# Kernel optimization log

Hardware: AMD Instinct MI355X
Metric: run time of the kernel (lower is better)

Reference implementation:

```python
import jax, jax.numpy as jnp
import numpy as np

N = 100000          # nodes
E = 1600000         # edges
IN_DIM = 128
HID = 64
N_CLASSES = 40
N_GAT_LAYERS = 2    # n_layers - 1
ALPHA = 0.2         # LeakyReLU slope
NEG_BIG = -9.0e15


def setup_inputs() -> dict:
    key = jax.random.key(0)
    ks = jax.random.split(key, 8)
    x = jax.random.normal(ks[0], (N, IN_DIM), dtype=jnp.float32)
    edge_index = jax.random.randint(ks[1], (2, E), 0, N, dtype=jnp.int64)
    # parameters (xavier-ish scale)
    emb_w = jax.random.normal(ks[2], (IN_DIM, HID), dtype=jnp.float32) * (1.414 / np.sqrt(IN_DIM + HID))
    emb_b = jnp.zeros((HID,), dtype=jnp.float32)
    Ws = jax.random.normal(ks[3], (N_GAT_LAYERS, HID, HID), dtype=jnp.float32) * (1.414 / np.sqrt(2 * HID))
    attn_a = jax.random.normal(ks[4], (N_GAT_LAYERS, 1, 2 * HID), dtype=jnp.float32) * (1.414 / np.sqrt(1 + 2 * HID))
    out_w = jax.random.normal(ks[5], (HID, N_CLASSES), dtype=jnp.float32) * (1.414 / np.sqrt(HID + N_CLASSES))
    out_b = jnp.zeros((N_CLASSES,), dtype=jnp.float32)
    return {"x": x, "edge_index": edge_index, "emb_w": emb_w, "emb_b": emb_b,
            "Ws": Ws, "attn_a": attn_a, "out_w": out_w, "out_b": out_b}


def _gat_conv(x, edge_src, edge_dst, W, a):
    # x: [N, d_in], W: [d_in, d_out], a: [1, 2*d_out]
    wh = x @ W                                   # [N, d_out]
    d = wh.shape[1]
    a_src = a[0, :d]                             # [d]
    a_dst = a[0, d:]                             # [d]
    # (a * cat(wh[src], wh[dst])).sum(1) == (wh @ a_src)[src] + (wh @ a_dst)[dst]
    s_src = wh @ a_src                           # [N]
    s_dst = wh @ a_dst                           # [N]
    e = jax.nn.leaky_relu(s_src[edge_src] + s_dst[edge_dst], negative_slope=ALPHA)  # [E]
    att = jnp.where(e > 0, e, NEG_BIG)
    att = jax.nn.softmax(att, axis=0)            # GLOBAL softmax over all edges (as in source)
    # scatter-aggregate weighted neighbor features into destination nodes
    msgs = att[:, None] * wh[edge_src]           # [E, d_out]
    h_prime = jax.ops.segment_sum(msgs, edge_dst, num_segments=wh.shape[0])  # [N, d_out]
    return jax.nn.elu(h_prime)                   # concat=True branch


def reference(x, edge_index, emb_w, emb_b, Ws, attn_a, out_w, out_b):
    edge_src = edge_index[0]
    edge_dst = edge_index[1]
    h = x @ emb_w + emb_b                        # emb Linear
    for l in range(N_GAT_LAYERS):
        h = _gat_conv(h, edge_src, edge_dst, Ws[l], attn_a[l])
    h = h @ out_w + out_b                        # out_att Linear
    h = jax.nn.elu(h)
    return jax.nn.log_softmax(h, axis=1)
```

## Files before the change

kernel.cpp:

```cpp
#include <hip/hip_runtime.h>
#include <hip/hip_bf16.h>

#define NODES   100000
#define EDGES   1600000
#define INDIM   128
#define HID     64
#define NCLS    40
#define NEG_BIG_F (-9000000000000000.0f)
#define SENTINEL  (-3.0e38f)

#define BN       512
#define NBUCK    196
#define CHUNK    7168
#define NCHUNK   ((EDGES + CHUNK - 1) / CHUNK)
#define BCAP     8960
#define MZPB     256
#define SMB      128

using bf16x8 = __attribute__((ext_vector_type(8))) short;
using f32x4  = __attribute__((ext_vector_type(4))) float;

static __device__ __forceinline__ float b2f(__hip_bfloat16 h){
    return __bfloat162float(h);
}
static __device__ __forceinline__ float bits2f(unsigned int b){
    union { unsigned int u; float f; } v; v.u = b << 16; return v.f;
}
static __device__ __forceinline__ unsigned short f2b(float f){
    __hip_bfloat16 h = __float2bfloat16(f);
    return *reinterpret_cast<unsigned short*>(&h);
}
static __device__ __forceinline__ float ldin(const void* p, int i, bool f32){
    return f32 ? ((const float*)p)[i] : b2f(((const __hip_bfloat16*)p)[i]);
}
static __device__ __forceinline__ float elu_fast(float x){
    return (x > 0.f) ? x : (__expf(x) - 1.f);
}
static __device__ __forceinline__ unsigned fenc(float f){
    unsigned u = __float_as_uint(f);
    return (u & 0x80000000u) ? ~u : (u | 0x80000000u);
}
static __device__ __forceinline__ float fdec(unsigned k){
    return __uint_as_float((k & 0x80000000u) ? (k & 0x7fffffffu) : ~k);
}
static __device__ __forceinline__ int ld_src(const int* ei, int i, bool i64){
    return i64 ? ei[2*i] : ei[i];
}
static __device__ __forceinline__ int ld_dst(const int* ei, int i, bool i64){
    return i64 ? ei[2*(EDGES + i)] : ei[EDGES + i];
}

__global__ __launch_bounds__(256) void k_detect(const unsigned* __restrict__ xw,
                                                const unsigned* __restrict__ eiw,
                                                int* __restrict__ flags){
    __shared__ int s1[256], s2[256];
    int t = threadIdx.x;
    int c1 = 0, c2 = 0;
    for(int i = t; i < 1024; i += 256){
        unsigned e = (xw[i] >> 23) & 0xffu;
        c1 += (e >= 90u && e <= 160u) ? 1 : 0;
        c2 += (eiw[2*i + 1] == 0u) ? 1 : 0;
    }
    s1[t] = c1; s2[t] = c2; __syncthreads();
    for(int off = 128; off > 0; off >>= 1){
        if(t < off){ s1[t] += s1[t+off]; s2[t] += s2[t+off]; }
        __syncthreads();
    }
    if(t == 0){ flags[0] = (s1[0] > 512) ? 1 : 0; flags[1] = (s2[0] > 512) ? 1 : 0; }
}

__global__ __launch_bounds__(256) void k_bhist(const int* __restrict__ ei,
                                               const int* __restrict__ flags,
                                               int* __restrict__ bdeg){
    __shared__ int sh[NBUCK];
    bool i64 = flags[1] != 0;
    int t = threadIdx.x;
    for(int i = t; i < NBUCK; i += 256) sh[i] = 0;
    __syncthreads();
    int i = blockIdx.x*256 + t;
    int stride = gridDim.x*256;
    for(; i < EDGES; i += stride) atomicAdd(&sh[ld_dst(ei, i, i64) >> 9], 1);
    __syncthreads();
    for(int b = t; b < NBUCK; b += 256) if(sh[b]) atomicAdd(&bdeg[b], sh[b]);
}

__global__ __launch_bounds__(256) void k_bscan(const int* __restrict__ bdeg,
                        int* __restrict__ bstart, int* __restrict__ bcursor){
    __shared__ int sh[256];
    int t = threadIdx.x;
    int v = (t < NBUCK) ? bdeg[t] : 0;
    sh[t] = v; __syncthreads();
    for(int off = 1; off < 256; off <<= 1){
        int x = (t >= off) ? sh[t - off] : 0;
        __syncthreads();
        sh[t] += x;
        __syncthreads();
    }
    int excl = sh[t] - v;
    if(t < NBUCK){ bstart[t] = excl; bcursor[t] = excl; }
    if(t == 255) bstart[NBUCK] = sh[255];
}

__global__ __launch_bounds__(256) void k_bucket_scatter(const int* __restrict__ ei,
    const int* __restrict__ flags, int* __restrict__ bcursor, int2* __restrict__ tmp){
    __shared__ int  sCnt[NBUCK], sScan[NBUCK], sCur[NBUCK], sGofs[NBUCK];
    __shared__ int2 stage[CHUNK];
    bool i64 = flags[1] != 0;
    int t = threadIdx.x;
    int base = blockIdx.x * CHUNK;
    int n = EDGES - base; if(n > CHUNK) n = CHUNK; if(n <= 0) return;

    for(int b = t; b < NBUCK; b += 256) sCnt[b] = 0;
    __syncthreads();
    for(int j = t; j < n; j += 256)
        atomicAdd(&sCnt[ld_dst(ei, base + j, i64) >> 9], 1);
    __syncthreads();
    for(int b = t; b < NBUCK; b += 256) sScan[b] = sCnt[b];
    __syncthreads();
    for(int off = 1; off < NBUCK; off <<= 1){
        int v = 0;
        if(t < NBUCK && t >= off) v = sScan[t - off];
        __syncthreads();
        if(t < NBUCK) sScan[t] += v;
        __syncthreads();
    }
    if(t < NBUCK){
        int excl = sScan[t] - sCnt[t];
        sCur[t]  = excl;
        sGofs[t] = sCnt[t] ? atomicAdd(&bcursor[t], sCnt[t]) : 0;
    }
    __syncthreads();
    for(int j = t; j < n; j += 256){
        int src = ld_src(ei, base + j, i64);
        int dst = ld_dst(ei, base + j, i64);
        int pos = atomicAdd(&sCur[dst >> 9], 1);
        stage[pos] = make_int2(src, dst);
    }
    __syncthreads();
    for(int i = t; i < n; i += 256){
        int2 e = stage[i];
        int  b = e.y >> 9;
        int  excl = sScan[b] - sCnt[b];
        tmp[(size_t)sGofs[b] + (i - excl)] = e;
    }
}

__global__ __launch_bounds__(512) void k_bucket_sort(const int2* __restrict__ tmp,
    const int* __restrict__ bstart, int* __restrict__ col,
    int* __restrict__ rowst){
    __shared__ int  sCnt[BN], sScan[BN], sCur[BN];
    __shared__ int2 stage[BCAP];
    int b = blockIdx.x, t = threadIdx.x;
    int nb0 = b * BN;
    int gbase = bstart[b], gend = bstart[b+1];
    int cnt = gend - gbase;

    if(t < BN) sCnt[t] = 0;
    __syncthreads();
    for(int j = gbase + t; j < gend; j += 512)
        atomicAdd(&sCnt[tmp[j].y - nb0], 1);
    __syncthreads();
    if(t < BN) sScan[t] = sCnt[t];
    __syncthreads();
    for(int off = 1; off < BN; off <<= 1){
        int v = 0;
        if(t < BN && t >= off) v = sScan[t - off];
        __syncthreads();
        if(t < BN) sScan[t] += v;
        __syncthreads();
    }
    if(t < BN) sCur[t] = sScan[t] - sCnt[t];
    if(t < BN && (nb0 + t) < NODES) rowst[nb0 + t] = gbase + (sScan[t] - sCnt[t]);
    if(b == 0 && t == 0) rowst[NODES] = EDGES;
    __syncthreads();
    for(int j = gbase + t; j < gend; j += 512){
        int2 e = tmp[j];
        int pos = atomicAdd(&sCur[e.y - nb0], 1);
        if(pos < BCAP) stage[pos] = e;
        else col[gbase + pos] = e.x;
    }
    __syncthreads();
    int lim = (cnt < BCAP) ? cnt : BCAP;
    for(int i = t; i < lim; i += 512)
        col[gbase + i] = stage[i].x;
}

template<int K, int AMODE, bool WITH_BIAS, bool WITH_SCORES, bool CBF16, int SCALEA>
__global__ __launch_bounds__(256) void k_gemm(
    const void* __restrict__ Aptr,
    const void* __restrict__ Wb,   int woff,
    const void* __restrict__ biasb,
    const void* __restrict__ attnb, int aoff,
    const int*  __restrict__ flags,
    void* __restrict__ Cout,
    float* __restrict__ s_src,
    float* __restrict__ s_dst,
    const float2* __restrict__ mzv,
    const float2* __restrict__ MZg)
{
    __shared__ short As[64][72];
    __shared__ short Bs[64][72];
    const bool wf32 = flags[0] != 0;
    const bool af32 = (AMODE == 2) ? true : ((AMODE == 3) ? false : wf32);
    const int t = threadIdx.x;
    const int block_row = blockIdx.x * 64;
    const int w  = t >> 6;
    const int l  = t & 63;
    const int srow = t >> 2;
    const int sq   = t & 3;
    const int grow_s = block_row + srow;

    float sA = 1.f;
    if constexpr (SCALEA == 1){
        float2 gz = MZg[0];
        float2 nm = (grow_s < NODES) ? mzv[grow_s] : make_float2(SENTINEL, 0.f);
        sA = __expf(nm.x - gz.x) * gz.y;
    }

    f32x4 acc[4] = { {0.f,0.f,0.f,0.f},{0.f,0.f,0.f,0.f},
                     {0.f,0.f,0.f,0.f},{0.f,0.f,0.f,0.f} };

    for(int kb = 0; kb < K; kb += 64){
        {
            unsigned o[16];
            if(af32){
                const float4* av4 = (const float4*)((const float*)Aptr + (size_t)grow_s*K + kb);
                #pragma unroll
                for(int i=0;i<4;i++){
                    float4 u = make_float4(0.f,0.f,0.f,0.f);
                    if(grow_s < NODES) u = av4[sq*4 + i];
                    if constexpr (SCALEA == 1){
                        u.x = elu_fast(u.x*sA); u.y = elu_fast(u.y*sA);
                        u.z = elu_fast(u.z*sA); u.w = elu_fast(u.w*sA);
                    }
                    o[4*i+0]=f2b(u.x); o[4*i+1]=f2b(u.y);
                    o[4*i+2]=f2b(u.z); o[4*i+3]=f2b(u.w);
                }
            } else {
                const uint4* avb = (const uint4*)((const unsigned short*)Aptr + (size_t)grow_s*K + kb);
                #pragma unroll
                for(int i=0;i<2;i++){
                    uint4 u = make_uint4(0,0,0,0);
                    if(grow_s < NODES) u = avb[sq*2 + i];
                    o[8*i+0]=u.x&0xffffu; o[8*i+1]=u.x>>16;
                    o[8*i+2]=u.y&0xffffu; o[8*i+3]=u.y>>16;
                    o[8*i+4]=u.z&0xffffu; o[8*i+5]=u.z>>16;
                    o[8*i+6]=u.w&0xffffu; o[8*i+7]=u.w>>16;
                }
            }
            uint4* dst = (uint4*)&As[srow][sq*16];
            dst[0] = make_uint4(o[0]|(o[1]<<16),  o[2]|(o[3]<<16),
                                o[4]|(o[5]<<16),  o[6]|(o[7]<<16));
            dst[1] = make_uint4(o[8]|(o[9]<<16),  o[10]|(o[11]<<16),
                                o[12]|(o[13]<<16),o[14]|(o[15]<<16));
        }
        if(wf32){
            const float* wv = (const float*)Wb + woff + (size_t)kb*64;
            #pragma unroll
            for(int i=0;i<16;i++){
                int idx = t + 256*i;
                Bs[idx & 63][idx >> 6] = (short)f2b(wv[idx]);
            }
        } else {
            const unsigned short* wv = (const unsigned short*)Wb + woff + (size_t)kb*64;
            #pragma unroll
            for(int i=0;i<16;i++){
                int idx = t + 256*i;
                Bs[idx & 63][idx >> 6] = (short)wv[idx];
            }
        }
        __syncthreads();
        #pragma unroll
        for(int s=0;s<2;s++){
            int k0 = s*32 + 8*(l >> 4);
            bf16x8 a = *(const bf16x8*)&As[16*w + (l & 15)][k0];
            #pragma unroll
            for(int c=0;c<4;c++){
                bf16x8 b = *(const bf16x8*)&Bs[16*c + (l & 15)][k0];
                acc[c] = __builtin_amdgcn_mfma_f32_16x16x32_bf16(a, b, acc[c], 0, 0, 0);
            }
        }
        __syncthreads();
    }

    const int lg4 = (l >> 4) * 4;
    const int lc  = l & 15;
    float bias[4] = {0.f,0.f,0.f,0.f};
    if constexpr (WITH_BIAS){
        #pragma unroll
        for(int c=0;c<4;c++) bias[c] = ldin(biasb, 16*c + lc, wf32);
    }
    #pragma unroll
    for(int r=0;r<4;r++){
        int grow = block_row + 16*w + lg4 + r;
        if(grow < NODES){
            #pragma unroll
            for(int c=0;c<4;c++){
                float vv = acc[c][r] + bias[c];
                if constexpr (CBF16)
                    ((unsigned short*)Cout)[(size_t)grow*64 + 16*c + lc] = f2b(vv);
                else
                    ((float*)Cout)[(size_t)grow*64 + 16*c + lc] = vv;
            }
        }
    }
    if constexpr (WITH_SCORES){
        float as_[4], ad_[4];
        #pragma unroll
        for(int c=0;c<4;c++){
            as_[c] = ldin(attnb, aoff + 16*c + lc, wf32);
            ad_[c] = ldin(attnb, aoff + 64 + 16*c + lc, wf32);
        }
        #pragma unroll
        for(int r=0;r<4;r++){
            float ps = 0.f, pd = 0.f;
            #pragma unroll
            for(int c=0;c<4;c++){
                ps = fmaf(acc[c][r], as_[c], ps);
                pd = fmaf(acc[c][r], ad_[c], pd);
            }
            ps += __shfl_xor(ps, 1, 64); pd += __shfl_xor(pd, 1, 64);
            ps += __shfl_xor(ps, 2, 64); pd += __shfl_xor(pd, 2, 64);
            ps += __shfl_xor(ps, 4, 64); pd += __shfl_xor(pd, 4, 64);
            ps += __shfl_xor(ps, 8, 64); pd += __shfl_xor(pd, 8, 64);
            int grow = block_row + 16*w + lg4 + r;
            if(lc == 0 && grow < NODES){ s_src[grow] = ps; s_dst[grow] = pd; }
        }
    }
}

__global__ __launch_bounds__(256) void k_smax(const float* __restrict__ ssrc,
                                              unsigned* __restrict__ smaxk){
    int tid = blockIdx.x*256 + threadIdx.x;
    int stride = gridDim.x*256;
    float m = SENTINEL;
    for(int i = tid; i < NODES; i += stride) m = fmaxf(m, ssrc[i]);
    #pragma unroll
    for(int off=1; off<64; off<<=1) m = fmaxf(m, __shfl_xor(m, off, 64));
    __shared__ float sm[4];
    int w = threadIdx.x >> 6;
    if((threadIdx.x & 63) == 0) sm[w] = m;
    __syncthreads();
    if(threadIdx.x == 0){
        for(int i=1;i<4;i++) m = fmaxf(m, sm[i]);
        atomicMax(smaxk, fenc(m));
    }
}

__global__ __launch_bounds__(256) void k_aggregate(const unsigned short* __restrict__ wh16,
    const int* __restrict__ row_start, const int* __restrict__ col,
    const float* __restrict__ ssrc, const float* __restrict__ sdst,
    const unsigned* __restrict__ smaxk,
    float* __restrict__ U, float2* __restrict__ mz)
{
    int gw = (blockIdx.x*256 + threadIdx.x) >> 3;
    if(gw >= NODES) return;
    int l8 = threadIdx.x & 7;
    int sb = (threadIdx.x & 63) & ~7;
    int c8 = l8 * 8;
    int beg = row_start[gw], end = row_start[gw+1];
    float sdn = sdst[gw];
    const float m = fdec(*smaxk) + sdn;
    float zl = 0.f;
    float acc[8] = {0.f,0.f,0.f,0.f,0.f,0.f,0.f,0.f};
    for(int base = beg; base < end; base += 16){
        int idx0 = base + l8;
        int idx1 = base + 8 + l8;
        bool v0 = idx0 < end, v1 = idx1 < end;
        int s0 = v0 ? col[idx0] : 0;
        int s1 = v1 ? col[idx1] : 0;
        float x0 = ssrc[s0] + sdn;
        float x1 = ssrc[s1] + sdn;
        float att0 = (v0 && x0 > 0.f) ? x0 : NEG_BIG_F;
        float att1 = (v1 && x1 > 0.f) ? x1 : NEG_BIG_F;
        float w0 = __expf(att0 - m);
        float w1 = __expf(att1 - m);
        zl += w0 + w1;
        #pragma unroll
        for(int j = 0; j < 8; j++){
            int   s = __shfl(s0, sb + j, 64);
            float a = __shfl(w0, sb + j, 64);
            uint4 u = *(const uint4*)&wh16[(size_t)s*64 + c8];
            acc[0] = fmaf(a, bits2f(u.x & 0xffffu), acc[0]);
            acc[1] = fmaf(a, bits2f(u.x >> 16),     acc[1]);
            acc[2] = fmaf(a, bits2f(u.y & 0xffffu), acc[2]);
            acc[3] = fmaf(a, bits2f(u.y >> 16),     acc[3]);
            acc[4] = fmaf(a, bits2f(u.z & 0xffffu), acc[4]);
            acc[5] = fmaf(a, bits2f(u.z >> 16),     acc[5]);
            acc[6] = fmaf(a, bits2f(u.w & 0xffffu), acc[6]);
            acc[7] = fmaf(a, bits2f(u.w >> 16),     acc[7]);
        }
        #pragma unroll
        for(int j = 0; j < 8; j++){
            int   s = __shfl(s1, sb + j, 64);
            float a = __shfl(w1, sb + j, 64);
            uint4 u = *(const uint4*)&wh16[(size_t)s*64 + c8];
            acc[0] = fmaf(a, bits2f(u.x & 0xffffu), acc[0]);
            acc[1] = fmaf(a, bits2f(u.x >> 16),     acc[1]);
            acc[2] = fmaf(a, bits2f(u.y & 0xffffu), acc[2]);
            acc[3] = fmaf(a, bits2f(u.y >> 16),     acc[3]);
            acc[4] = fmaf(a, bits2f(u.z & 0xffffu), acc[4]);
            acc[5] = fmaf(a, bits2f(u.z >> 16),     acc[5]);
            acc[6] = fmaf(a, bits2f(u.w & 0xffffu), acc[6]);
            acc[7] = fmaf(a, bits2f(u.w >> 16),     acc[7]);
        }
    }
    zl += __shfl_xor(zl, 1, 64);
    zl += __shfl_xor(zl, 2, 64);
    zl += __shfl_xor(zl, 4, 64);
    if(l8 == 0) mz[gw] = make_float2(m, zl);
    *(float4*)&U[(size_t)gw*64 + c8 + 0] = make_float4(acc[0],acc[1],acc[2],acc[3]);
    *(float4*)&U[(size_t)gw*64 + c8 + 4] = make_float4(acc[4],acc[5],acc[6],acc[7]);
}

__global__ __launch_bounds__(256) void k_mz_part(const float2* __restrict__ mz,
                                                 float2* __restrict__ bmz){
    int tid = blockIdx.x*256 + threadIdx.x;
    int stride = gridDim.x*256;
    float m = SENTINEL, z = 0.f;
    for(int i = tid; i < NODES; i += stride){
        float2 e = mz[i];
        float M = fmaxf(m, e.x);
        z = z*__expf(m - M) + e.y*__expf(e.x - M);
        m = M;
    }
    for(int off=1; off<64; off<<=1){
        float m2 = __shfl_xor(m, off, 64), z2 = __shfl_xor(z, off, 64);
        float M = fmaxf(m, m2);
        z = z*__expf(m - M) + z2*__expf(m2 - M);
        m = M;
    }
    __shared__ float sm[4], sz[4];
    int w = threadIdx.x >> 6;
    if((threadIdx.x & 63) == 0){ sm[w] = m; sz[w] = z; }
    __syncthreads();
    if(threadIdx.x == 0){
        for(int i=1;i<4;i++){
            float M = fmaxf(m, sm[i]);
            z = z*__expf(m - M) + sz[i]*__expf(sm[i] - M);
            m = M;
        }
        bmz[blockIdx.x] = make_float2(m, z);
    }
}

__global__ __launch_bounds__(256) void k_mz_final(const float2* __restrict__ bmz,
                                                  float2* __restrict__ MZ,
                                                  unsigned* __restrict__ smaxk){
    int t = threadIdx.x;
    float m = SENTINEL, z = 0.f;
    for(int i = t; i < MZPB; i += 256){
        float2 e = bmz[i];
        float M = fmaxf(m, e.x);
        z = z*__expf(m - M) + e.y*__expf(e.x - M);
        m = M;
    }
    for(int off=1; off<64; off<<=1){
        float m2 = __shfl_xor(m, off, 64), z2 = __shfl_xor(z, off, 64);
        float M = fmaxf(m, m2);
        z = z*__expf(m - M) + z2*__expf(m2 - M);
        m = M;
    }
    __shared__ float sm[4], sz[4];
    int w = t >> 6;
    if((t & 63) == 0){ sm[w] = m; sz[w] = z; }
    __syncthreads();
    if(t == 0){
        for(int i=1;i<4;i++){
            float M = fmaxf(m, sm[i]);
            z = z*__expf(m - M) + sz[i]*__expf(sm[i] - M);
            m = M;
        }
        MZ[0] = make_float2(m, 1.0f / z);
        smaxk[0] = 0u;
    }
}

__global__ __launch_bounds__(256) void k_out(const float* __restrict__ h,
    const float2* __restrict__ mzv, const float2* __restrict__ MZg,
    const void* __restrict__ Wo, const void* __restrict__ bo,
    const int* __restrict__ flags, float* __restrict__ out)
{
    __shared__ float Ht[64][65];
    __shared__ float Wsh[64][44];
    __shared__ float logits[64][44];
    __shared__ float rlz[64];
    bool f32 = flags[0] != 0;
    int t = threadIdx.x;
    int block_row = blockIdx.x * 64;

    for(int i = t; i < 64*NCLS; i += 256){
        Wsh[i/NCLS][i%NCLS] = ldin(Wo, i, f32);
    }
    {
        int r_load = t >> 2, q = t & 3;
        int grow = block_row + r_load;
        const float4* hv = (const float4*)h;
        float2 gz = MZg[0];
        float2 nm = (grow < NODES) ? mzv[grow] : make_float2(SENTINEL, 0.f);
        float sA = __expf(nm.x - gz.x) * gz.y;
        #pragma unroll
        for(int i = 0; i < 4; i++){
            int vi = q + 4*i;
            float4 u = make_float4(0.f,0.f,0.f,0.f);
            if(grow < NODES) u = hv[(size_t)grow*16 + vi];
            u.x = elu_fast(u.x*sA); u.y = elu_fast(u.y*sA);
            u.z = elu_fast(u.z*sA); u.w = elu_fast(u.w*sA);
            Ht[vi*4+0][r_load] = u.x; Ht[vi*4+1][r_load] = u.y;
            Ht[vi*4+2][r_load] = u.z; Ht[vi*4+3][r_load] = u.w;
        }
    }
    __syncthreads();

    int cg = t & 15, rg = t >> 4;
    int c0 = cg * 4, r0 = rg * 4;
    if(cg < 10){
        float acc[4][4] = {{0.f,0.f,0.f,0.f},{0.f,0.f,0.f,0.f},{0.f,0.f,0.f,0.f},{0.f,0.f,0.f,0.f}};
        #pragma unroll 8
        for(int k = 0; k < 64; k++){
            float4 a = *(const float4*)&Ht[k][r0];
            float4 w = *(const float4*)&Wsh[k][c0];
            float av4[4] = {a.x,a.y,a.z,a.w};
            float wv4[4] = {w.x,w.y,w.z,w.w};
            #pragma unroll
            for(int i=0;i<4;i++)
                #pragma unroll
                for(int j=0;j<4;j++)
                    acc[i][j] = fmaf(av4[i], wv4[j], acc[i][j]);
        }
        float b[4];
        #pragma unroll
        for(int j=0;j<4;j++) b[j] = ldin(bo, c0+j, f32);
        #pragma unroll
        for(int i=0;i<4;i++)
            #pragma unroll
            for(int j=0;j<4;j++){
                logits[r0+i][c0+j] = elu_fast(acc[i][j] + b[j]);
            }
    }
    __syncthreads();

    {
        int r = t >> 2, qq = t & 3;
        float m = SENTINEL;
        #pragma unroll
        for(int i=0;i<10;i++) m = fmaxf(m, logits[r][qq*10 + i]);
        m = fmaxf(m, __shfl_xor(m, 1, 64));
        m = fmaxf(m, __shfl_xor(m, 2, 64));
        float s = 0.f;
        #pragma unroll
        for(int i=0;i<10;i++) s += __expf(logits[r][qq*10 + i] - m);
        s += __shfl_xor(s, 1, 64);
        s += __shfl_xor(s, 2, 64);
        if(qq == 0) rlz[r] = m + logf(s);
    }
    __syncthreads();

    for(int i = t; i < 64*NCLS; i += 256){
        int rr = i / NCLS, cc = i % NCLS;
        if(block_row + rr < NODES)
            out[(size_t)(block_row)*NCLS + i] = logits[rr][cc] - rlz[rr];
    }
}

extern "C" void kernel_launch(void* const* d_in, const int* in_sizes, int n_in,
                              void* d_out, int out_size, void* d_ws, size_t ws_size,
                              hipStream_t stream)
{
    const void* x      = d_in[0];
    const int*  ei     = (const int*)d_in[1];
    const void* emb_w  = d_in[2];
    const void* emb_b  = d_in[3];
    const void* Ws     = d_in[4];
    const void* attn_a = d_in[5];
    const void* out_w  = d_in[6];
    const void* out_b  = d_in[7];
    float* out = (float*)d_out;

    char* ws = (char*)d_ws;
    size_t off = 0;
    auto alloc = [&](size_t bytes)->char*{
        char* p = ws + off;
        off = (off + bytes + 255) & ~(size_t)255;
        return p;
    };
    int*    flags   = (int*)   alloc(256);
    float*  h       = (float*) alloc((size_t)NODES*HID*4);
    unsigned short* h0 = (unsigned short*)alloc((size_t)NODES*HID*2);
    unsigned short* wh16 = (unsigned short*)alloc((size_t)NODES*HID*2);
    float*  ssrc    = (float*) alloc((size_t)NODES*4);
    float*  sdst    = (float*) alloc((size_t)NODES*4);
    int*    rowst   = (int*)   alloc((size_t)(NODES+1)*4);
    int*    col     = (int*)   alloc((size_t)EDGES*4);
    float2* mz      = (float2*)alloc((size_t)NODES*8);
    int*    bdeg    = (int*)   alloc(NBUCK*4);
    int*    bstart  = (int*)   alloc((NBUCK+1)*4);
    int*    bcursor = (int*)   alloc(NBUCK*4);
    float2* bmz     = (float2*)alloc(MZPB*8);
    float2* MZ      = (float2*)alloc(16);
    unsigned* smaxk = (unsigned*)alloc(256);

    int2* tmp = (int2*)h;

    k_detect<<<1, 256, 0, stream>>>((const unsigned*)x, (const unsigned*)ei, flags);

    hipMemsetAsync(bdeg, 0, NBUCK*4, stream);
    hipMemsetAsync(smaxk, 0, 4, stream);
    k_bhist<<<256, 256, 0, stream>>>(ei, flags, bdeg);
    k_bscan<<<1, 256, 0, stream>>>(bdeg, bstart, bcursor);
    k_bucket_scatter<<<NCHUNK, 256, 0, stream>>>(ei, flags, bcursor, tmp);
    k_bucket_sort<<<NBUCK, 512, 0, stream>>>(tmp, bstart, col, rowst);

    k_gemm<INDIM, 0, true, false, true, 0><<<(NODES+63)/64, 256, 0, stream>>>(
        x, emb_w, 0, emb_b, nullptr, 0, flags, h0, nullptr, nullptr, nullptr, nullptr);

    k_gemm<HID, 3, false, true, true, 0><<<(NODES+63)/64, 256, 0, stream>>>(
        h0, Ws, 0, nullptr, attn_a, 0, flags, wh16, ssrc, sdst, nullptr, nullptr);
    k_smax<<<SMB, 256, 0, stream>>>(ssrc, smaxk);
    k_aggregate<<<(NODES*8 + 255)/256, 256, 0, stream>>>(wh16, rowst, col, ssrc, sdst, smaxk, h, mz);
    k_mz_part <<<MZPB, 256, 0, stream>>>(mz, bmz);
    k_mz_final<<<1, 256, 0, stream>>>(bmz, MZ, smaxk);

    k_gemm<HID, 2, false, true, true, 1><<<(NODES+63)/64, 256, 0, stream>>>(
        h, Ws, HID*HID, nullptr, attn_a, 2*HID, flags, wh16, ssrc, sdst, mz, MZ);
    k_smax<<<SMB, 256, 0, stream>>>(ssrc, smaxk);
    k_aggregate<<<(NODES*8 + 255)/256, 256, 0, stream>>>(wh16, rowst, col, ssrc, sdst, smaxk, h, mz);
    k_mz_part <<<MZPB, 256, 0, stream>>>(mz, bmz);
    k_mz_final<<<1, 256, 0, stream>>>(bmz, MZ, smaxk);

    k_out<<<(NODES+63)/64, 256, 0, stream>>>(h, mz, MZ, out_w, out_b, flags, out);
}
```

Measured before the change: 306.6 us.

## Replace bucket sort with atomic counting CSR and fold softmax normalizer via dst max

CSR construction switches from a two-pass bucket scatter/sort with shared-memory staging to per-node degree atomics, a block row scan, and a direct atomic-cursor scatter of sources. The global softmax normalizer now uses the global max of destination scores as the reference, so each aggregate block emits a partial sum and a single small kernel finishes it. This replaces the per-node (m,z) array and the two-stage log-sum-exp reduction. The unnormalized aggregate is stored in bf16 instead of fp32, with ELU and scaling applied on load in the next GEMM. The change trades memory traffic and launches for more global atomics, a non-deterministic column order within rows, and bf16 rounding of intermediates.

Result: slower. 464.7 us (+51.6%).

```diff
diff --git a/kernel.cpp b/kernel.cpp
--- a/kernel.cpp
+++ b/kernel.cpp
@@ -11,10 +11,7 @@
 
 #define BN       512
 #define NBUCK    196
-#define CHUNK    7168
-#define NCHUNK   ((EDGES + CHUNK - 1) / CHUNK)
-#define BCAP     8960
-#define MZPB     256
+#define AGB      3125
 #define SMB      128
 
 using bf16x8 = __attribute__((ext_vector_type(8))) short;
@@ -71,6 +68,7 @@
 
 __global__ __launch_bounds__(256) void k_bhist(const int* __restrict__ ei,
                                                const int* __restrict__ flags,
+                                               int* __restrict__ deg,
                                                int* __restrict__ bdeg){
     __shared__ int sh[NBUCK];
     bool i64 = flags[1] != 0;
@@ -79,13 +77,17 @@
     __syncthreads();
     int i = blockIdx.x*256 + t;
     int stride = gridDim.x*256;
-    for(; i < EDGES; i += stride) atomicAdd(&sh[ld_dst(ei, i, i64) >> 9], 1);
+    for(; i < EDGES; i += stride){
+        int d = ld_dst(ei, i, i64);
+        atomicAdd(&deg[d], 1);
+        atomicAdd(&sh[d >> 9], 1);
+    }
     __syncthreads();
     for(int b = t; b < NBUCK; b += 256) if(sh[b]) atomicAdd(&bdeg[b], sh[b]);
 }
 
 __global__ __launch_bounds__(256) void k_bscan(const int* __restrict__ bdeg,
-                        int* __restrict__ bstart, int* __restrict__ bcursor){
+                                               int* __restrict__ bstart){
     __shared__ int sh[256];
     int t = threadIdx.x;
     int v = (t < NBUCK) ? bdeg[t] : 0;
@@ -96,93 +98,38 @@
         sh[t] += x;
         __syncthreads();
     }
-    int excl = sh[t] - v;
-    if(t < NBUCK){ bstart[t] = excl; bcursor[t] = excl; }
-    if(t == 255) bstart[NBUCK] = sh[255];
-}
-
-__global__ __launch_bounds__(256) void k_bucket_scatter(const int* __restrict__ ei,
-    const int* __restrict__ flags, int* __restrict__ bcursor, int2* __restrict__ tmp){
-    __shared__ int  sCnt[NBUCK], sScan[NBUCK], sCur[NBUCK], sGofs[NBUCK];
-    __shared__ int2 stage[CHUNK];
+    if(t < NBUCK) bstart[t] = sh[t] - v;
+}
+
+__global__ __launch_bounds__(512) void k_rowscan(const int* __restrict__ deg,
+    const int* __restrict__ bstart, int* __restrict__ rowst, int* __restrict__ cursor){
+    __shared__ int sScan[BN];
+    int b = blockIdx.x, t = threadIdx.x;
+    int n = b*BN + t;
+    int v = (n < NODES) ? deg[n] : 0;
+    sScan[t] = v; __syncthreads();
+    for(int off = 1; off < BN; off <<= 1){
+        int x = (t >= off) ? sScan[t - off] : 0;
+        __syncthreads();
+        sScan[t] += x;
+        __syncthreads();
+    }
+    int r = bstart[b] + (sScan[t] - v);
+    if(n < NODES){ rowst[n] = r; cursor[n] = r; }
+    if(b == 0 && t == 0) rowst[NODES] = EDGES;
+}
+
+__global__ __launch_bounds__(256) void k_scatter(const int* __restrict__ ei,
+    const int* __restrict__ flags, int* __restrict__ cursor, int* __restrict__ col){
     bool i64 = flags[1] != 0;
-    int t = threadIdx.x;
-    int base = blockIdx.x * CHUNK;
-    int n = EDGES - base; if(n > CHUNK) n = CHUNK; if(n <= 0) return;
-
-    for(int b = t; b < NBUCK; b += 256) sCnt[b] = 0;
-    __syncthreads();
-    for(int j = t; j < n; j += 256)
-        atomicAdd(&sCnt[ld_dst(ei, base + j, i64) >> 9], 1);
-    __syncthreads();
-    for(int b = t; b < NBUCK; b += 256) sScan[b] = sCnt[b];
-    __syncthreads();
-    for(int off = 1; off < NBUCK; off <<= 1){
-        int v = 0;
-        if(t < NBUCK && t >= off) v = sScan[t - off];
-        __syncthreads();
-        if(t < NBUCK) sScan[t] += v;
-        __syncthreads();
-    }
-    if(t < NBUCK){
-        int excl = sScan[t] - sCnt[t];
-        sCur[t]  = excl;
-        sGofs[t] = sCnt[t] ? atomicAdd(&bcursor[t], sCnt[t]) : 0;
-    }
-    __syncthreads();
-    for(int j = t; j < n; j += 256){
-        int src = ld_src(ei, base + j, i64);
-        int dst = ld_dst(ei, base + j, i64);
-        int pos = atomicAdd(&sCur[dst >> 9], 1);
-        stage[pos] = make_int2(src, dst);
-    }
-    __syncthreads();
-    for(int i = t; i < n; i += 256){
-        int2 e = stage[i];
-        int  b = e.y >> 9;
-        int  excl = sScan[b] - sCnt[b];
-        tmp[(size_t)sGofs[b] + (i - excl)] = e;
-    }
-}
-
-__global__ __launch_bounds__(512) void k_bucket_sort(const int2* __restrict__ tmp,
-    const int* __restrict__ bstart, int* __restrict__ col,
-    int* __restrict__ rowst){
-    __shared__ int  sCnt[BN], sScan[BN], sCur[BN];
-    __shared__ int2 stage[BCAP];
-    int b = blockIdx.x, t = threadIdx.x;
-    int nb0 = b * BN;
-    int gbase = bstart[b], gend = bstart[b+1];
-    int cnt = gend - gbase;
-
-    if(t < BN) sCnt[t] = 0;
-    __syncthreads();
-    for(int j = gbase + t; j < gend; j += 512)
-        atomicAdd(&sCnt[tmp[j].y - nb0], 1);
-    __syncthreads();
-    if(t < BN) sScan[t] = sCnt[t];
-    __syncthreads();
-    for(int off = 1; off < BN; off <<= 1){
-        int v = 0;
-        if(t < BN && t >= off) v = sScan[t - off];
-        __syncthreads();
-        if(t < BN) sScan[t] += v;
-        __syncthreads();
-    }
-    if(t < BN) sCur[t] = sScan[t] - sCnt[t];
-    if(t < BN && (nb0 + t) < NODES) rowst[nb0 + t] = gbase + (sScan[t] - sCnt[t]);
-    if(b == 0 && t == 0) rowst[NODES] = EDGES;
-    __syncthreads();
-    for(int j = gbase + t; j < gend; j += 512){
-        int2 e = tmp[j];
-        int pos = atomicAdd(&sCur[e.y - nb0], 1);
-        if(pos < BCAP) stage[pos] = e;
-        else col[gbase + pos] = e.x;
-    }
-    __syncthreads();
-    int lim = (cnt < BCAP) ? cnt : BCAP;
-    for(int i = t; i < lim; i += 512)
-        col[gbase + i] = stage[i].x;
+    int i = blockIdx.x*256 + threadIdx.x;
+    int stride = gridDim.x*256;
+    for(; i < EDGES; i += stride){
+        int src = ld_src(ei, i, i64);
+        int dst = ld_dst(ei, i, i64);
+        int pos = atomicAdd(&cursor[dst], 1);
+        col[pos] = src;
+    }
 }
 
 template<int K, int AMODE, bool WITH_BIAS, bool WITH_SCORES, bool CBF16, int SCALEA>
@@ -195,7 +142,7 @@
     void* __restrict__ Cout,
     float* __restrict__ s_src,
     float* __restrict__ s_dst,
-    const float2* __restrict__ mzv,
+    const float* __restrict__ sdstv,
     const float2* __restrict__ MZg)
 {
     __shared__ short As[64][72];
@@ -213,8 +160,8 @@
     float sA = 1.f;
     if constexpr (SCALEA == 1){
         float2 gz = MZg[0];
-        float2 nm = (grow_s < NODES) ? mzv[grow_s] : make_float2(SENTINEL, 0.f);
-        sA = __expf(nm.x - gz.x) * gz.y;
+        float sd = (grow_s < NODES) ? sdstv[grow_s] : 0.f;
+        sA = __expf(sd - gz.x) * gz.y;
     }
 
     f32x4 acc[4] = { {0.f,0.f,0.f,0.f},{0.f,0.f,0.f,0.f},
@@ -242,10 +189,14 @@
                 for(int i=0;i<2;i++){
                     uint4 u = make_uint4(0,0,0,0);
                     if(grow_s < NODES) u = avb[sq*2 + i];
-                    o[8*i+0]=u.x&0xffffu; o[8*i+1]=u.x>>16;
-                    o[8*i+2]=u.y&0xffffu; o[8*i+3]=u.y>>16;
-                    o[8*i+4]=u.z&0xffffu; o[8*i+5]=u.z>>16;
-                    o[8*i+6]=u.w&0xffffu; o[8*i+7]=u.w>>16;
+                    unsigned raw[8] = {u.x&0xffffu, u.x>>16, u.y&0xffffu, u.y>>16,
+                                       u.z&0xffffu, u.z>>16, u.w&0xffffu, u.w>>16};
+                    if constexpr (SCALEA == 1){
+                        #pragma unroll
+                        for(int j=0;j<8;j++) raw[j] = f2b(elu_fast(bits2f(raw[j])*sA));
+                    }
+                    #pragma unroll
+                    for(int j=0;j<8;j++) o[8*i+j] = raw[j];
                 }
             }
             uint4* dst = (uint4*)&As[srow][sq*16];
@@ -330,31 +281,39 @@
 }
 
 __global__ __launch_bounds__(256) void k_smax(const float* __restrict__ ssrc,
-                                              unsigned* __restrict__ smaxk){
+                                              const float* __restrict__ sdst,
+                                              unsigned* __restrict__ smaxk,
+                                              unsigned* __restrict__ dmaxk){
     int tid = blockIdx.x*256 + threadIdx.x;
     int stride = gridDim.x*256;
-    float m = SENTINEL;
-    for(int i = tid; i < NODES; i += stride) m = fmaxf(m, ssrc[i]);
+    float m1 = SENTINEL, m2 = SENTINEL;
+    for(int i = tid; i < NODES; i += stride){
+        m1 = fmaxf(m1, ssrc[i]);
+        m2 = fmaxf(m2, sdst[i]);
+    }
     #pragma unroll
-    for(int off=1; off<64; off<<=1) m = fmaxf(m, __shfl_xor(m, off, 64));
-    __shared__ float sm[4];
+    for(int off=1; off<64; off<<=1){
+        m1 = fmaxf(m1, __shfl_xor(m1, off, 64));
+        m2 = fmaxf(m2, __shfl_xor(m2, off, 64));
+    }
+    __shared__ float sm1[4], sm2[4];
     int w = threadIdx.x >> 6;
-    if((threadIdx.x & 63) == 0) sm[w] = m;
+    if((threadIdx.x & 63) == 0){ sm1[w] = m1; sm2[w] = m2; }
     __syncthreads();
     if(threadIdx.x == 0){
-        for(int i=1;i<4;i++) m = fmaxf(m, sm[i]);
-        atomicMax(smaxk, fenc(m));
+        for(int i=1;i<4;i++){ m1 = fmaxf(m1, sm1[i]); m2 = fmaxf(m2, sm2[i]); }
+        atomicMax(smaxk, fenc(m1));
+        atomicMax(dmaxk, fenc(m2));
     }
 }
 
 __global__ __launch_bounds__(256) void k_aggregate(const unsigned short* __restrict__ wh16,
     const int* __restrict__ row_start, const int* __restrict__ col,
     const float* __restrict__ ssrc, const float* __restrict__ sdst,
-    const unsigned* __restrict__ smaxk,
-    float* __restrict__ U, float2* __restrict__ mz)
+    const unsigned* __restrict__ smaxk, const unsigned* __restrict__ dmaxk,
+    unsigned short* __restrict__ U16, float* __restrict__ zpart)
 {
     int gw = (blockIdx.x*256 + threadIdx.x) >> 3;
-    if(gw >= NODES) return;
     int l8 = threadIdx.x & 7;
     int sb = (threadIdx.x & 63) & ~7;
     int c8 = l8 * 8;
@@ -408,76 +367,43 @@
     zl += __shfl_xor(zl, 1, 64);
     zl += __shfl_xor(zl, 2, 64);
     zl += __shfl_xor(zl, 4, 64);
-    if(l8 == 0) mz[gw] = make_float2(m, zl);
-    *(float4*)&U[(size_t)gw*64 + c8 + 0] = make_float4(acc[0],acc[1],acc[2],acc[3]);
-    *(float4*)&U[(size_t)gw*64 + c8 + 4] = make_float4(acc[4],acc[5],acc[6],acc[7]);
-}
-
-__global__ __launch_bounds__(256) void k_mz_part(const float2* __restrict__ mz,
-                                                 float2* __restrict__ bmz){
-    int tid = blockIdx.x*256 + threadIdx.x;
-    int stride = gridDim.x*256;
-    float m = SENTINEL, z = 0.f;
-    for(int i = tid; i < NODES; i += stride){
-        float2 e = mz[i];
-        float M = fmaxf(m, e.x);
-        z = z*__expf(m - M) + e.y*__expf(e.x - M);
-        m = M;
-    }
-    for(int off=1; off<64; off<<=1){
-        float m2 = __shfl_xor(m, off, 64), z2 = __shfl_xor(z, off, 64);
-        float M = fmaxf(m, m2);
-        z = z*__expf(m - M) + z2*__expf(m2 - M);
-        m = M;
-    }
-    __shared__ float sm[4], sz[4];
-    int w = threadIdx.x >> 6;
-    if((threadIdx.x & 63) == 0){ sm[w] = m; sz[w] = z; }
-    __syncthreads();
-    if(threadIdx.x == 0){
-        for(int i=1;i<4;i++){
-            float M = fmaxf(m, sm[i]);
-            z = z*__expf(m - M) + sz[i]*__expf(sm[i] - M);
-            m = M;
-        }
-        bmz[blockIdx.x] = make_float2(m, z);
-    }
-}
-
-__global__ __launch_bounds__(256) void k_mz_final(const float2* __restrict__ bmz,
-                                                  float2* __restrict__ MZ,
-                                                  unsigned* __restrict__ smaxk){
+    float zc = (l8 == 0) ? zl * __expf(sdn - fdec(*dmaxk)) : 0.f;
+    zc += __shfl_xor(zc, 8, 64);
+    zc += __shfl_xor(zc, 16, 64);
+    zc += __shfl_xor(zc, 32, 64);
+    __shared__ float zsh[4];
+    if((threadIdx.x & 63) == 0) zsh[threadIdx.x >> 6] = zc;
+    __syncthreads();
+    if(threadIdx.x == 0) zpart[blockIdx.x] = zsh[0]+zsh[1]+zsh[2]+zsh[3];
+    ushort4 o0 = make_ushort4(f2b(acc[0]), f2b(acc[1]), f2b(acc[2]), f2b(acc[3]));
+    ushort4 o1 = make_ushort4(f2b(acc[4]), f2b(acc[5]), f2b(acc[6]), f2b(acc[7]));
+    *(ushort4*)&U16[(size_t)gw*64 + c8 + 0] = o0;
+    *(ushort4*)&U16[(size_t)gw*64 + c8 + 4] = o1;
+}
+
+__global__ __launch_bounds__(256) void k_zfin(const float* __restrict__ zpart,
+                                              float2* __restrict__ MZ,
+                                              unsigned* __restrict__ smaxk,
+                                              unsigned* __restrict__ dmaxk){
     int t = threadIdx.x;
-    float m = SENTINEL, z = 0.f;
-    for(int i = t; i < MZPB; i += 256){
-        float2 e = bmz[i];
-        float M = fmaxf(m, e.x);
-        z = z*__expf(m - M) + e.y*__expf(e.x - M);
-        m = M;
-    }
-    for(int off=1; off<64; off<<=1){
-        float m2 = __shfl_xor(m, off, 64), z2 = __shfl_xor(z, off, 64);
-        float M = fmaxf(m, m2);
-        z = z*__expf(m - M) + z2*__expf(m2 - M);
-        m = M;
-    }
-    __shared__ float sm[4], sz[4];
+    float z = 0.f;
+    for(int i = t; i < AGB; i += 256) z += zpart[i];
+    #pragma unroll
+    for(int off=1; off<64; off<<=1) z += __shfl_xor(z, off, 64);
+    __shared__ float sz[4];
     int w = t >> 6;
-    if((t & 63) == 0){ sm[w] = m; sz[w] = z; }
+    if((t & 63) == 0) sz[w] = z;
     __syncthreads();
     if(t == 0){
-        for(int i=1;i<4;i++){
-            float M = fmaxf(m, sm[i]);
-            z = z*__expf(m - M) + sz[i]*__expf(sm[i] - M);
-            m = M;
-        }
-        MZ[0] = make_float2(m, 1.0f / z);
+        z = sz[0]+sz[1]+sz[2]+sz[3];
+        MZ[0] = make_float2(fdec(*dmaxk), 1.0f / z);
         smaxk[0] = 0u;
-    }
-}
-
-__global__ __launch_bounds__(256) void k_out(const float* __restrict__ h,
-    const float2* __restrict__ mzv, const float2* __restrict__ MZg,
+        dmaxk[0] = 0u;
+    }
+}
+
+__global__ __launch_bounds__(256) void k_out(const unsigned short* __restrict__ h16,
+    const float* __restrict__ sdstv, const float2* __restrict__ MZg,
     const void* __restrict__ Wo, const void* __restrict__ bo,
     const int* __restrict__ flags, float* __restrict__ out)
 {
@@ -495,19 +421,21 @@
     {
         int r_load = t >> 2, q = t & 3;
         int grow = block_row + r_load;
-        const float4* hv = (const float4*)h;
         float2 gz = MZg[0];
-        float2 nm = (grow < NODES) ? mzv[grow] : make_float2(SENTINEL, 0.f);
-        float sA = __expf(nm.x - gz.x) * gz.y;
-        #pragma unroll
-        for(int i = 0; i < 4; i++){
-            int vi = q + 4*i;
-            float4 u = make_float4(0.f,0.f,0.f,0.f);
-            if(grow < NODES) u = hv[(size_t)grow*16 + vi];
-            u.x = elu_fast(u.x*sA); u.y = elu_fast(u.y*sA);
-            u.z = elu_fast(u.z*sA); u.w = elu_fast(u.w*sA);
-            Ht[vi*4+0][r_load] = u.x; Ht[vi*4+1][r_load] = u.y;
-            Ht[vi*4+2][r_load] = u.z; Ht[vi*4+3][r_load] = u.w;
+        float sd = (grow < NODES) ? sdstv[grow] : 0.f;
+        float sA = __expf(sd - gz.x) * gz.y;
+        const uint4* hv = (const uint4*)h16;
+        #pragma unroll
+        for(int i = 0; i < 2; i++){
+            uint4 u = make_uint4(0,0,0,0);
+            if(grow < NODES) u = hv[(size_t)grow*8 + q*2 + i];
+            float f[8] = {bits2f(u.x&0xffffu), bits2f(u.x>>16),
+                          bits2f(u.y&0xffffu), bits2f(u.y>>16),
+                          bits2f(u.z&0xffffu), bits2f(u.z>>16),
+                          bits2f(u.w&0xffffu), bits2f(u.w>>16)};
+            int k0 = q*16 + i*8;
+            #pragma unroll
+            for(int j=0;j<8;j++) Ht[k0+j][r_load] = elu_fast(f[j]*sA);
         }
     }
     __syncthreads();
@@ -585,48 +513,46 @@
         return p;
     };
     int*    flags   = (int*)   alloc(256);
-    float*  h       = (float*) alloc((size_t)NODES*HID*4);
-    unsigned short* h0 = (unsigned short*)alloc((size_t)NODES*HID*2);
+    unsigned short* U16  = (unsigned short*)alloc((size_t)NODES*HID*2);
+    unsigned short* h0   = (unsigned short*)alloc((size_t)NODES*HID*2);
     unsigned short* wh16 = (unsigned short*)alloc((size_t)NODES*HID*2);
     float*  ssrc    = (float*) alloc((size_t)NODES*4);
-    float*  sdst    = (float*) alloc((size_t)NODES*4);
+    float*  sdstA   = (float*) alloc((size_t)NODES*4);
+    float*  sdstB   = (float*) alloc((size_t)NODES*4);
     int*    rowst   = (int*)   alloc((size_t)(NODES+1)*4);
+    int*    cursor  = (int*)   alloc((size_t)NODES*4);
+    int*    deg     = (int*)   alloc((size_t)NODES*4);
     int*    col     = (int*)   alloc((size_t)EDGES*4);
-    float2* mz      = (float2*)alloc((size_t)NODES*8);
     int*    bdeg    = (int*)   alloc(NBUCK*4);
     int*    bstart  = (int*)   alloc((NBUCK+1)*4);
-    int*    bcursor = (int*)   alloc(NBUCK*4);
-    float2* bmz     = (float2*)alloc(MZPB*8);
+    float*  zpart   = (float*) alloc(AGB*4);
     float2* MZ      = (float2*)alloc(16);
-    unsigned* smaxk = (unsigned*)alloc(256);
-
-    int2* tmp = (int2*)h;
+    unsigned* maxk  = (unsigned*)alloc(256);
 
     k_detect<<<1, 256, 0, stream>>>((const unsigned*)x, (const unsigned*)ei, flags);
 
+    hipMemsetAsync(deg,  0, (size_t)NODES*4, stream);
     hipMemsetAsync(bdeg, 0, NBUCK*4, stream);
-    hipMemsetAsync(smaxk, 0, 4, stream);
-    k_bhist<<<256, 256, 0, stream>>>(ei, flags, bdeg);
-    k_bscan<<<1, 256, 0, stream>>>(bdeg, bstart, bcursor);
-    k_bucket_scatter<<<NCHUNK, 256, 0, stream>>>(ei, flags, bcursor, tmp);
-    k_bucket_sort<<<NBUCK, 512, 0, stream>>>(tmp, bstart, col, rowst);
+    hipMemsetAsync(maxk, 0, 8, stream);
+    k_bhist  <<<256, 256, 0, stream>>>(ei, flags, deg, bdeg);
+    k_bscan  <<<1, 256, 0, stream>>>(bdeg, bstart);
+    k_rowscan<<<NBUCK, BN, 0, stream>>>(deg, bstart, rowst, cursor);
+    k_scatter<<<2048, 256, 0, stream>>>(ei, flags, cursor, col);
 
     k_gemm<INDIM, 0, true, false, true, 0><<<(NODES+63)/64, 256, 0, stream>>>(
         x, emb_w, 0, emb_b, nullptr, 0, flags, h0, nullptr, nullptr, nullptr, nullptr);
 
     k_gemm<HID, 3, false, true, true, 0><<<(NODES+63)/64, 256, 0, stream>>>(
-        h0, Ws, 0, nullptr, attn_a, 0, flags, wh16, ssrc, sdst, nullptr, nullptr);
-    k_smax<<<SMB, 256, 0, stream>>>(ssrc, smaxk);
-    k_aggregate<<<(NODES*8 + 255)/256, 256, 0, stream>>>(wh16, rowst, col, ssrc, sdst, smaxk, h, mz);
-    k_mz_part <<<MZPB, 256, 0, stream>>>(mz, bmz);
-    k_mz_final<<<1, 256, 0, stream>>>(bmz, MZ, smaxk);
-
-    k_gemm<HID, 2, false, true, true, 1><<<(NODES+63)/64, 256, 0, stream>>>(
-        h, Ws, HID*HID, nullptr, attn_a, 2*HID, flags, wh16, ssrc, sdst, mz, MZ);
-    k_smax<<<SMB, 256, 0, stream>>>(ssrc, smaxk);
-    k_aggregate<<<(NODES*8 + 255)/256, 256, 0, stream>>>(wh16, rowst, col, ssrc, sdst, smaxk, h, mz);
-    k_mz_part <<<MZPB, 256, 0, stream>>>(mz, bmz);
-    k_mz_final<<<1, 256, 0, stream>>>(bmz, MZ, smaxk);
-
-    k_out<<<(NODES+63)/64, 256, 0, stream>>>(h, mz, MZ, out_w, out_b, flags, out);
-}
+        h0, Ws, 0, nullptr, attn_a, 0, flags, wh16, ssrc, sdstA, nullptr, nullptr);
+    k_smax<<<SMB, 256, 0, stream>>>(ssrc, sdstA, maxk, maxk+1);
+    k_aggregate<<<AGB, 256, 0, stream>>>(wh16, rowst, col, ssrc, sdstA, maxk, maxk+1, U16, zpart);
+    k_zfin<<<1, 256, 0, stream>>>(zpart, MZ, maxk, maxk+1);
+
+    k_gemm<HID, 3, false, true, true, 1><<<(NODES+63)/64, 256, 0, stream>>>(
+        U16, Ws, HID*HID, nullptr, attn_a, 2*HID, flags, wh16, ssrc, sdstB, sdstA, MZ);
+    k_smax<<<SMB, 256, 0, stream>>>(ssrc, sdstB, maxk, maxk+1);
+    k_aggregate<<<AGB, 256, 0, stream>>>(wh16, rowst, col, ssrc, sdstB, maxk, maxk+1, U16, zpart);
+    k_zfin<<<1, 256, 0, stream>>>(zpart, MZ, maxk, maxk+1);
+
+    k_out<<<(NODES+63)/64, 256, 0, stream>>>(U16, sdstB, MZ, out_w, out_b, flags, out);
+}
```
